# Optimization experiments

Measured on AMD Instinct MI355X. Metric: run time of the kernel, lower is better.

The kernel has to match this reference:

```python
import jax, jax.numpy as jnp
import numpy as np

N = 12288
E = 196608
H = 128
Z = 128
NEG = -1e9  # finite mask value (avoids -inf NaNs in grads)
WSCALE = 0.05


def setup_inputs() -> dict:
    key = jax.random.key(0)
    ks = jax.random.split(key, 16)
    inp = {}
    inp["x"] = jax.random.normal(ks[0], (N, 2), dtype=jnp.float32)
    inp["z"] = jax.random.normal(ks[1], (Z,), dtype=jnp.float32)
    inp["node_type"] = jax.random.randint(ks[2], (N,), 0, 3, dtype=jnp.int32)
    inp["node_depth"] = jax.random.randint(ks[3], (N,), 0, 64, dtype=jnp.int32)
    inp["edge_index"] = jax.random.randint(ks[4], (2, E), 0, N, dtype=jnp.int32)
    inp["W1"] = jax.random.normal(ks[5], (2, H), dtype=jnp.float32) * WSCALE
    inp["b1"] = jnp.zeros((H,), jnp.float32)
    inp["W2"] = jax.random.normal(ks[6], (H, H), dtype=jnp.float32) * WSCALE
    inp["b2"] = jnp.zeros((H,), jnp.float32)
    inp["Wm1"] = jax.random.normal(ks[7], (H + Z, H), dtype=jnp.float32) * WSCALE
    inp["bm1"] = jnp.zeros((H,), jnp.float32)
    inp["Wm2"] = jax.random.normal(ks[8], (H, H), dtype=jnp.float32) * WSCALE
    inp["bm2"] = jnp.zeros((H,), jnp.float32)
    inp["Ws"] = jax.random.normal(ks[9], (H, H), dtype=jnp.float32) * WSCALE
    inp["Wt"] = jax.random.normal(ks[10], (H, H), dtype=jnp.float32) * WSCALE
    inp["Wi1"] = jax.random.normal(ks[11], (2 * H + Z, H), dtype=jnp.float32) * WSCALE
    inp["bi1"] = jnp.zeros((H,), jnp.float32)
    inp["Wi2"] = jax.random.normal(ks[12], (H, 1), dtype=jnp.float32) * WSCALE
    inp["bi2"] = jnp.zeros((1,), jnp.float32)
    return inp


def _gcn(x, W, b, src, dst, n):
    # GCNConv with self-loops and symmetric deg^-1/2 normalization
    loop = jnp.arange(n, dtype=src.dtype)
    s = jnp.concatenate([src, loop])
    d = jnp.concatenate([dst, loop])
    deg = jax.ops.segment_sum(jnp.ones_like(d, dtype=x.dtype), d, num_segments=n)
    inv_sqrt = jnp.where(deg > 0, jax.lax.rsqrt(jnp.maximum(deg, 1.0)), 0.0)
    w = inv_sqrt[s] * inv_sqrt[d]  # [E+N]
    agg = jax.ops.segment_sum(x[s] * w[:, None], d, num_segments=n)  # [N,F]
    return agg @ W + b


def reference(x, z, node_type, node_depth, edge_index,
              W1, b1, W2, b2, Wm1, bm1, Wm2, bm2, Ws, Wt, Wi1, bi1, Wi2, bi2):
    n = x.shape[0]
    src, dst = edge_index[0], edge_index[1]
    # 2-layer GCN encode
    h = jax.nn.relu(_gcn(x, W1, b1, src, dst, n))
    h = jax.nn.relu(_gcn(h, W2, b2, src, dst, n))
    # node_mlp on [h, z] (no outer relu, per original edge_index branch)
    zb = jnp.broadcast_to(z, (n, Z))
    h = jax.nn.relu(jnp.concatenate([h, zb], axis=1) @ Wm1 + bm1) @ Wm2 + bm2  # [N,H]
    # batched score: St[v,u] = tgt_proj(h_v) . src_proj(h_u)
    St = (h @ Wt) @ (h @ Ws).T  # [N(target), N(candidate)]
    cand_ok = node_depth[None, :] < node_depth[:, None]  # candidate strictly shallower
    St = jnp.where(cand_ok, St, NEG)
    vals, idx = jax.lax.top_k(St, 2)  # [N,2] per-target top candidates
    # target is active if type != 0, depth > 0, and at least one candidate exists
    tv = (node_type != 0) & (node_depth > 0) & (vals[:, 0] > NEG / 2)
    # k=2 edges for AND nodes (type==2), else k=1
    edge_valid = jnp.stack([tv, tv & (node_type == 2)], axis=1)  # [N,2]
    # inversion bit mlp on [h_u, h_v, z]
    hu = h[idx]  # [N,2,H]
    hv = jnp.broadcast_to(h[:, None, :], hu.shape)
    zz = jnp.broadcast_to(z, (n, 2, Z))
    feat = jnp.concatenate([hu, hv, zz], axis=-1)  # [N,2,2H+Z]
    logit = (jax.nn.relu(feat @ Wi1 + bi1) @ Wi2 + bi2)[..., 0]  # [N,2]
    inv_prob = jax.nn.sigmoid(logit)
    return inv_prob, vals, idx, edge_valid
```

## Files before the change

### kernel.cpp

```cpp
#include <hip/hip_runtime.h>
#include <hip/hip_bf16.h>

#define NN 12288
#define NE 196608
#define HD 128
#define ZD 128
#define NEGV (-1.0e9f)
#define SEG 16

using s8v = __attribute__((ext_vector_type(8))) short;
using f4v = __attribute__((ext_vector_type(4))) float;
using i4v = __attribute__((ext_vector_type(4))) int;

__device__ __forceinline__ unsigned short f2bf(float f) {
    return __builtin_bit_cast(unsigned short, __float2bfloat16(f));
}
__device__ __forceinline__ float4 pack8(float4 a, float4 b) {
    unsigned p0 = ((unsigned)f2bf(a.y) << 16) | f2bf(a.x);
    unsigned p1 = ((unsigned)f2bf(a.w) << 16) | f2bf(a.z);
    unsigned p2 = ((unsigned)f2bf(b.y) << 16) | f2bf(b.x);
    unsigned p3 = ((unsigned)f2bf(b.w) << 16) | f2bf(b.z);
    i4v r = (i4v){(int)p0, (int)p1, (int)p2, (int)p3};
    return __builtin_bit_cast(float4, r);
}
// ... 126 lines not shown
    __shared__ int lh[64];
    __shared__ int lbase[64];
    int tid = threadIdx.x;
    if (blockIdx.x < NE / 256) {
        int e = blockIdx.x * 256 + tid;
        int u = esrc[e], v = edst[e];
        int pos = atomicAdd(&cursor[v], 1);
        ebsrc[pos] = u;
        ebw[pos] = inv[u] * inv[v];
    } else {
        if (tid < 64) lh[tid] = 0;
        __syncthreads();
        int v = (blockIdx.x - NE / 256) * 256 + tid;
        int d = ndep[v];
        int r = atomicAdd(&lh[d], 1);
        __syncthreads();
        if (tid < 64) {
            int c = lh[tid];
            if (c) lbase[tid] = atomicAdd(&dcur[tid * 16], c);
        }
        __syncthreads();
        int p = lbase[d] + r;
        sidx[p] = v;
        sdep[p] = d;
        prank[v] = p;
    }
}

__global__ __launch_bounds__(256) void k_gather2(const int* __restrict__ offs,
                                                 const int* __restrict__ ebsrc,
                                                 const float* __restrict__ ebw,
                                                 const float* __restrict__ x,
                                                 float* agg2) {
    int v = blockIdx.x * 256 + threadIdx.x;
    float ax = agg2[2 * v], ay = agg2[2 * v + 1];
    int b = offs[v], e = offs[v + 1];
    const float2* X2 = (const float2*)x;
    int k = b;
    for (; k + 4 <= e; k += 4) {
        int u0 = ebsrc[k], u1 = ebsrc[k + 1], u2 = ebsrc[k + 2], u3 = ebsrc[k + 3];
        float w0 = ebw[k], w1 = ebw[k + 1], w2 = ebw[k + 2], w3 = ebw[k + 3];
        float2 x0 = X2[u0], x1 = X2[u1], x2 = X2[u2], x3 = X2[u3];
        ax = fmaf(x0.x, w0, ax); ay = fmaf(x0.y, w0, ay);
        ax = fmaf(x1.x, w1, ax); ay = fmaf(x1.y, w1, ay);
        ax = fmaf(x2.x, w2, ax); ay = fmaf(x2.y, w2, ay);
        ax = fmaf(x3.x, w3, ax); ay = fmaf(x3.y, w3, ay);
    }
    for (; k < e; ++k) {
        int u = ebsrc[k];
        float w = ebw[k];
        float2 xv = X2[u];
        ax = fmaf(xv.x, w, ax);
        ay = fmaf(xv.y, w, ay);
    }
    agg2[2 * v] = ax;
    agg2[2 * v + 1] = ay;
}

__global__ __launch_bounds__(256) void k_lin1(const float* __restrict__ agg2,
                                              const float* __restrict__ W1,
                                              const float* __restrict__ b1,
                                              const float* __restrict__ inv,
                                              unsigned short* h1b, float* aggH) {
    int t = blockIdx.x * 256 + threadIdx.x;
    int v = t >> 7, j = t & 127;
    float hv = fmaxf(fmaf(agg2[2 * v], W1[j],
                     fmaf(agg2[2 * v + 1], W1[HD + j], b1[j])), 0.f);
    h1b[t] = f2bf(hv);
    float iv = inv[v];
    aggH[t] = hv * iv * iv;
}

__global__ __launch_bounds__(256) void k_gatherH(const int* __restrict__ offs,
                                                 const int* __restrict__ ebsrc,
                                                 const float* __restrict__ ebw,
                                                 const unsigned short* __restrict__ h1b,
                                                 float* aggH) {
    int tid = threadIdx.x;
    int lane = tid & 63;
    int v = blockIdx.x * 4 + (tid >> 6);
    const unsigned* H1 = (const unsigned*)h1b;
    float2* A2 = (float2*)aggH;
    float2 acc = A2[(size_t)v * 64 + lane];
    int b = offs[v], e = offs[v + 1];
    int k = b;
    for (; k + 4 <= e; k += 4) {
        int u0 = ebsrc[k], u1 = ebsrc[k + 1], u2 = ebsrc[k + 2], u3 = ebsrc[k + 3];
        float w0 = ebw[k], w1 = ebw[k + 1], w2 = ebw[k + 2], w3 = ebw[k + 3];
        unsigned hb0 = H1[(size_t)u0 * 64 + lane];
// ... 108 lines not shown
        const float4* wt = wt4 + 2 * 2048;
        NBACC(wt, col0, cA) NBACC(wt, col1, cB)
        float q0 = bbm2[col0], q1 = bbm2[col1];
        LDS4(cA, q0, col0, usB) LDS4(cB, q1, col1, usB)
    }
    __syncthreads();
    {
        AFRAGS(bufB4)
        const float4* wt = wt4 + 3 * 2048;
        NBACC(wt, col0, cA) NBACC(wt, col1, cB)
        GBF4S(cA, col0, htb) GBF4S(cB, col1, htb)
    }
    {
        AFRAGS(bufB4)
        const float4* wt = wt4 + 4 * 2048;
        NBACC(wt, col0, cA) NBACC(wt, col1, cB)
        GBF4S(cA, col0, hsb) GBF4S(cB, col1, hsb)
    }
    {
        AFRAGS(bufB4)
        const float4* wt = wt4 + 5 * 2048;
        NBACC(wt, col0, cA) NBACC(wt, col1, cB)
        GF4(cA, 0.f, col0, outA) GF4(cB, 0.f, col1, outA)
    }
    {
        AFRAGS(bufB4)
        const float4* wt = wt4 + 6 * 2048;
        NBACC(wt, col0, cA) NBACC(wt, col1, cB)
        float q0 = bcz2[col0], q1 = bcz2[col1];
        GF4(cA, q0, col0, outB) GF4(cB, q1, col1, outB)
    }
}

#define STG(buf, q, val) { int r_ = (q) >> 4, c_ = (q) & 15; \
    (buf)[r_ * 16 + (c_ ^ (r_ & 7))] = (val); }

#define KC2(kc, AX, AY) { \
    int co_ = (kc) * 4 + quad; \
    int bo_ = bbase + (co_ ^ brm); \
    s8v b0_ = __builtin_bit_cast(s8v, B[bo_      ]); \
    s8v b1_ = __builtin_bit_cast(s8v, B[bo_ + 256]); \
    s8v b2_ = __builtin_bit_cast(s8v, B[bo_ + 512]); \
    s8v b3_ = __builtin_bit_cast(s8v, B[bo_ + 768]); \
    x0 = __builtin_amdgcn_mfma_f32_16x16x32_bf16(AX, b0_, x0, 0, 0, 0); \
    y0 = __builtin_amdgcn_mfma_f32_16x16x32_bf16(AY, b0_, y0, 0, 0, 0); \
    x1 = __builtin_amdgcn_mfma_f32_16x16x32_bf16(AX, b1_, x1, 0, 0, 0); \
    y1 = __builtin_amdgcn_mfma_f32_16x16x32_bf16(AY, b1_, y1, 0, 0, 0); \
    x2 = __builtin_amdgcn_mfma_f32_16x16x32_bf16(AX, b2_, x2, 0, 0, 0); \
    y2 = __builtin_amdgcn_mfma_f32_16x16x32_bf16(AY, b2_, y2, 0, 0, 0); \
    x3 = __builtin_amdgcn_mfma_f32_16x16x32_bf16(AX, b3_, x3, 0, 0, 0); \
    y3 = __builtin_amdgcn_mfma_f32_16x16x32_bf16(AY, b3_, y3, 0, 0, 0); }

#define RMG(K1, K2, EL, DV) { \
    unsigned pb_ = (__builtin_bit_cast(unsigned, EL) & 0xFFFFC000u) | e_; \
    float sf_ = __builtin_bit_cast(float, (du_ < (DV)) ? pb_ : negp_); \
    K2 = __builtin_amdgcn_fmed3f(K1, K2, sf_); \
    K1 = fmaxf(K1, sf_); }

#define MGEN(nb, XA, YA) { \
    int p_ = u0 + (nb) * 16 + lane16; \
    int du_ = sdep[p_]; \
    unsigned e_ = 0x3FFFu - (unsigned)sidx[p_]; \
    unsigned negp_ = negbase | e_; \
    RMG(k1x0, k2x0, XA[0], dvx0) RMG(k1x1, k2x1, XA[1], dvx1) \
    RMG(k1x2, k2x2, XA[2], dvx2) RMG(k1x3, k2x3, XA[3], dvx3) \
    RMG(k1y0, k2y0, YA[0], dvy0) RMG(k1y1, k2y1, YA[1], dvy1) \
    RMG(k1y2, k2y2, YA[2], dvy2) RMG(k1y3, k2y3, YA[3], dvy3) }

#define RMF(K1, K2, EL) { \
    float sf_ = __builtin_bit_cast(float, \
        (__builtin_bit_cast(unsigned, EL) & 0xFFFFC000u) | e_); \
    K2 = __builtin_amdgcn_fmed3f(K1, K2, sf_); \
    K1 = fmaxf(K1, sf_); }

#define MFAST(nb, XA, YA) { \
    int p_ = u0 + (nb) * 16 + lane16; \
    unsigned e_ = 0x3FFFu - (unsigned)sidx[p_]; \
    RMF(k1x0, k2x0, XA[0]) RMF(k1x1, k2x1, XA[1]) \
    RMF(k1x2, k2x2, XA[2]) RMF(k1x3, k2x3, XA[3]) \
    RMF(k1y0, k2y0, YA[0]) RMF(k1y1, k2y1, YA[1]) \
    RMF(k1y2, k2y2, YA[2]) RMF(k1y3, k2y3, YA[3]) }

#define BF1(K1, K2, m) { \
    float o1_ = __shfl_xor(K1, m, 64); \
    float o2_ = __shfl_xor(K2, m, 64); \
    float m2_ = fmaxf(K2, o2_); \
    K2 = __builtin_amdgcn_fmed3f(K1, o1_, m2_); \
    K1 = fmaxf(K1, o1_); }

#define BFALL(m) \
    BF1(k1x0, k2x0, m) BF1(k1x1, k2x1, m) BF1(k1x2, k2x2, m) BF1(k1x3, k2x3, m) \
    BF1(k1y0, k2y0, m) BF1(k1y1, k2y1, m) BF1(k1y2, k2y2, m) BF1(k1y3, k2y3, m)

#define EMIT2(K1, K2, GROW) { \
    size_t o = ((size_t)seg * NN + (GROW)) * 2; \
    pv[o] = K1; pv[o + 1] = K2; }

__global__ __launch_bounds__(256) void k_score_top2_mfma(
        const __hip_bfloat16* __restrict__ htb,
        const __hip_bfloat16* __restrict__ hsb,
        const int* __restrict__ sdep, const int* __restrict__ sidx,
        const int* __restrict__ bofs,
        float* __restrict__ pv) {
    __shared__ float4 Bs4[2][64 * 16];
    int tid = threadIdx.x;
    int w = tid >> 6;
    int l = tid & 63;
    int lane16 = l & 15;
    int quad = l >> 4;
    int rb = (int)gridDim.x - 1 - (int)blockIdx.x;
    int row0 = rb * 128;
    int seg = blockIdx.y;
    const unsigned negbase = __builtin_bit_cast(unsigned, NEGV) & 0xFFFFC000u;

    int dmax = sdep[row0 + 127];
    int lim = bofs[dmax];
    int nt = (lim + 63) >> 6;
    int ns = (nt + 11) / 12;
    if (ns < 1) ns = 1;
    if (seg >= ns) {
        if (tid < 128) {
            int grow = sidx[row0 + tid];
            size_t o = ((size_t)seg * NN + grow) * 2;
            pv[o]     = __builtin_bit_cast(float, negbase | 0x3FFFu);
            pv[o + 1] = __builtin_bit_cast(float, negbase | 0x3FFEu);
        }
        return;
    }
    int t0 = (seg * nt) / ns;
    int t1 = ((seg + 1) * nt) / ns;

    int rbase = row0 + w * 32;
    s8v ax0, ax1, ax2, ax3, ay0, ay1, ay2, ay3;
    {
        const float4* gx = (const float4*)(htb + (size_t)(rbase + lane16) * HD);
        ax0 = __builtin_bit_cast(s8v, gx[quad]);
        ax1 = __builtin_bit_cast(s8v, gx[4 + quad]);
        ax2 = __builtin_bit_cast(s8v, gx[8 + quad]);
        ax3 = __builtin_bit_cast(s8v, gx[12 + quad]);
        const float4* gy = (const float4*)(htb + (size_t)(rbase + 16 + lane16) * HD);
        ay0 = __builtin_bit_cast(s8v, gy[quad]);
        ay1 = __builtin_bit_cast(s8v, gy[4 + quad]);
        ay2 = __builtin_bit_cast(s8v, gy[8 + quad]);
        ay3 = __builtin_bit_cast(s8v, gy[12 + quad]);
    }
    if (t0 < t1) {
        float4* B0 = Bs4[t0 & 1];
        const float4* gb = (const float4*)(hsb + (size_t)(t0 * 64) * HD);
        float4 b0_ = gb[tid], b1_ = gb[tid + 256], b2_ = gb[tid + 512], b3_ = gb[tid + 768];
        STG(B0, tid, b0_) STG(B0, tid + 256, b1_)
        STG(B0, tid + 512, b2_) STG(B0, tid + 768, b3_)
    }

    int bbase = lane16 * 16, brm = lane16 & 7;

    int dvx0 = sdep[rbase + quad * 4 + 0];
    int dvx1 = sdep[rbase + quad * 4 + 1];
    int dvx2 = sdep[rbase + quad * 4 + 2];
    int dvx3 = sdep[rbase + quad * 4 + 3];
    int dvy0 = sdep[rbase + 16 + quad * 4 + 0];
    int dvy1 = sdep[rbase + 16 + quad * 4 + 1];
    int dvy2 = sdep[rbase + 16 + quad * 4 + 2];
    int dvy3 = sdep[rbase + 16 + quad * 4 + 3];
    int lim_lo = bofs[sdep[rbase]];
    int lim_hi = bofs[sdep[rbase + 31]];

    float ki1 = (lane16 == 0) ? __builtin_bit_cast(float, negbase | 0x3FFFu) : -3.4e38f;
    float ki2 = (lane16 == 0) ? __builtin_bit_cast(float, negbase | 0x3FFEu) : -3.4e38f;
    float k1x0 = ki1, k1x1 = ki1, k1x2 = ki1, k1x3 = ki1;
    float k1y0 = ki1, k1y1 = ki1, k1y2 = ki1, k1y3 = ki1;
    float k2x0 = ki2, k2x1 = ki2, k2x2 = ki2, k2x3 = ki2;
    float k2y0 = ki2, k2y1 = ki2, k2y2 = ki2, k2y3 = ki2;

    float4 p0, p1, p2, p3;
    for (int t = t0; t < t1; ++t) {
        int u0 = t * 64;
        __syncthreads();
        if (t + 1 < t1) {
            const float4* g = (const float4*)(hsb + (size_t)(u0 + 64) * HD);
            p0 = g[tid]; p1 = g[tid + 256]; p2 = g[tid + 512]; p3 = g[tid + 768];
        }
        if (u0 < lim_hi) {
            const float4* B = Bs4[t & 1];
            f4v x0 = (f4v){0.f, 0.f, 0.f, 0.f};
            f4v x1 = (f4v){0.f, 0.f, 0.f, 0.f};
            f4v x2 = (f4v){0.f, 0.f, 0.f, 0.f};
            f4v x3 = (f4v){0.f, 0.f, 0.f, 0.f};
            f4v y0 = (f4v){0.f, 0.f, 0.f, 0.f};
            f4v y1 = (f4v){0.f, 0.f, 0.f, 0.f};
            f4v y2 = (f4v){0.f, 0.f, 0.f, 0.f};
            f4v y3 = (f4v){0.f, 0.f, 0.f, 0.f};
            KC2(0, ax0, ay0) KC2(1, ax1, ay1) KC2(2, ax2, ay2) KC2(3, ax3, ay3)
            if (u0 + 64 <= lim_lo) {
                MFAST(0, x0, y0) MFAST(1, x1, y1)
                MFAST(2, x2, y2) MFAST(3, x3, y3)
            } else {
                MGEN(0, x0, y0) MGEN(1, x1, y1)
                MGEN(2, x2, y2) MGEN(3, x3, y3)
            }
        }
        if (t + 1 < t1) {
            float4* Bn = Bs4[(t + 1) & 1];
            STG(Bn, tid, p0) STG(Bn, tid + 256, p1)
            STG(Bn, tid + 512, p2) STG(Bn, tid + 768, p3)
        }
    }

    BFALL(1) BFALL(2) BFALL(4) BFALL(8)

    if (lane16 == 0) {
        int gbse = rbase + quad * 4;
        EMIT2(k1x0, k2x0, sidx[gbse + 0])
        EMIT2(k1x1, k2x1, sidx[gbse + 1])
        EMIT2(k1x2, k2x2, sidx[gbse + 2])
        EMIT2(k1x3, k2x3, sidx[gbse + 3])
        EMIT2(k1y0, k2y0, sidx[gbse + 16])
        EMIT2(k1y1, k2y1, sidx[gbse + 17])
        EMIT2(k1y2, k2y2, sidx[gbse + 18])
        EMIT2(k1y3, k2y3, sidx[gbse + 19])
    }
}

__global__ __launch_bounds__(256) void k_final(const float* __restrict__ pv,
                                               const int* __restrict__ ntype,
                                               const int* __restrict__ ndepth,
                                               const float* __restrict__ A,
                                               const float* __restrict__ B,
                                               const float* __restrict__ Wi2,
                                               const float* __restrict__ bi2,
                                               float* __restrict__ out) {
    int tid = threadIdx.x;
    int lane = tid & 63;
    int v = blockIdx.x * 4 + (tid >> 6);

    float k1 = -3.4e38f;
    if (lane < 32) {
        k1 = pv[((size_t)(lane >> 1) * NN + v) * 2 + (lane & 1)];
    }
    float k2 = -3.4e38f;
#pragma unroll
    for (int m = 1; m <= 16; m <<= 1) {
        float o1 = __shfl_xor(k1, m, 64);
        float o2 = __shfl_xor(k2, m, 64);
        float m2 = fmaxf(k2, o2);
        k2 = __builtin_amdgcn_fmed3f(k1, o1, m2);
        k1 = fmaxf(k1, o1);
    }
    float K1 = __shfl(k1, 0, 64);
    float K2 = __shfl(k2, 0, 64);
    unsigned b1 = __builtin_bit_cast(unsigned, K1);
    unsigned b2 = __builtin_bit_cast(unsigned, K2);
    int I1 = 0x3FFF - (int)(b1 & 0x3FFFu);
// ... 67 lines not shown
    int*   pi     = (int*)(pv + S2N);
    int*   cnt    = pi;
    int*   dcur   = pi + 1024;
    int*   degi   = pi + S2N;
    float* inv    = (float*)(degi + NN + 64);
    float* agg2   = inv + NN;
    float* cz1    = agg2 + 2 * NN;
    float* cz2    = cz1 + 128;
    int*   offs   = (int*)(cz2 + 128);
    int*   cursor = offs + NN + 16;
    int*   bofs   = cursor + NN;
    int*   sidx   = bofs + 80 + 64;
    int*   sdep   = sidx + NN;
    int*   prank  = sdep + NN;
    int*   ebsrc  = prank + NN;
    float* ebw    = (float*)(ebsrc + NE);
    __hip_bfloat16* wt7 = (__hip_bfloat16*)(ebw + NE);
    size_t F = (size_t)NN * HD;
    float* s0 = (float*)(wt7 + 7 * 16384);
    float* s1 = s0 + F;
    float* s2 = s1 + F;
    unsigned short* h1b = (unsigned short*)s0;
    __hip_bfloat16* htb = (__hip_bfloat16*)s0;
    __hip_bfloat16* hsb = htb + F;

    hipMemsetAsync(degi, 0, NN * sizeof(int), stream);
    hipMemsetAsync(cnt, 0, 1024 * sizeof(int), stream);
    k_counts_wz<<<NE / 256 + NN / 256 + 448 + 1, 256, 0, stream>>>(
        edst, ndep, W2, Wm1, Wm2, Wtm, Wsm, Wi1, z, bm1, bi1,
        degi, cnt, wt7, cz1, cz2);
    k_prefix<<<1, 1024, 0, stream>>>(degi, cnt, x, inv, agg2, offs, cursor, bofs, dcur);
    k_bucket_scatter<<<NE / 256 + NN / 256, 256, 0, stream>>>(
        esrc, edst, ndep, inv, cursor, ebsrc, ebw, dcur, sidx, sdep, prank);
    k_gather2<<<NN / 256, 256, 0, stream>>>(offs, ebsrc, ebw, x, agg2);
    k_lin1<<<NN * HD / 256, 256, 0, stream>>>(agg2, W1, b1, inv, h1b, s1);
    k_gatherH<<<NN / 4, 256, 0, stream>>>(offs, ebsrc, ebw, h1b, s1);
    k_mlp7_mfma<<<NN / 16, 256, 0, stream>>>(s1, wt7, b2, cz1, bm2, cz2,
                                             prank, s2, s1, htb, hsb);
    k_score_top2_mfma<<<dim3(NN / 128, SEG), 256, 0, stream>>>(
        htb, hsb, sdep, sidx, bofs, pv);
    k_final<<<NN / 4, 256, 0, stream>>>(pv, ntype, ndep, s2, s1, Wi2, bi2, out);
}
```

Baseline: 229.2 us.

## Double rows per wave in score/top2 kernel and stage candidate depth/index in LDS

Each wave of the score-and-top-2 kernel now handles 64 target rows instead of 32, so each block covers 256 rows and the grid halves. Every candidate B fragment read from shared memory now feeds twice as many MFMAs, cutting LDS traffic per unit of work. Candidate depth and index are also packed once per segment into a shared array, replacing the global sdep/sidx reads done inside the merge loop. The cost is roughly double the accumulator and top-2 register state, which may lower occupancy or cause spills, and fewer blocks in the grid.

Result: slower. 254.0 us (+10.8%).

```diff
diff --git a/kernel.cpp b/kernel.cpp
--- a/kernel.cpp
+++ b/kernel.cpp
@@ -382,21 +382,29 @@
 #define STG(buf, q, val) { int r_ = (q) >> 4, c_ = (q) & 15; \
     (buf)[r_ * 16 + (c_ ^ (r_ & 7))] = (val); }
 
-#define KC2(kc, AX, AY) { \
+#define MFMA_ __builtin_amdgcn_mfma_f32_16x16x32_bf16
+
+#define KC4(kc, AA, AB, AC, AD) { \
     int co_ = (kc) * 4 + quad; \
     int bo_ = bbase + (co_ ^ brm); \
     s8v b0_ = __builtin_bit_cast(s8v, B[bo_      ]); \
     s8v b1_ = __builtin_bit_cast(s8v, B[bo_ + 256]); \
     s8v b2_ = __builtin_bit_cast(s8v, B[bo_ + 512]); \
     s8v b3_ = __builtin_bit_cast(s8v, B[bo_ + 768]); \
-    x0 = __builtin_amdgcn_mfma_f32_16x16x32_bf16(AX, b0_, x0, 0, 0, 0); \
-    y0 = __builtin_amdgcn_mfma_f32_16x16x32_bf16(AY, b0_, y0, 0, 0, 0); \
-    x1 = __builtin_amdgcn_mfma_f32_16x16x32_bf16(AX, b1_, x1, 0, 0, 0); \
-    y1 = __builtin_amdgcn_mfma_f32_16x16x32_bf16(AY, b1_, y1, 0, 0, 0); \
-    x2 = __builtin_amdgcn_mfma_f32_16x16x32_bf16(AX, b2_, x2, 0, 0, 0); \
-    y2 = __builtin_amdgcn_mfma_f32_16x16x32_bf16(AY, b2_, y2, 0, 0, 0); \
-    x3 = __builtin_amdgcn_mfma_f32_16x16x32_bf16(AX, b3_, x3, 0, 0, 0); \
-    y3 = __builtin_amdgcn_mfma_f32_16x16x32_bf16(AY, b3_, y3, 0, 0, 0); }
+    accA0 = MFMA_(AA, b0_, accA0, 0, 0, 0); accB0 = MFMA_(AB, b0_, accB0, 0, 0, 0); \
+    accC0 = MFMA_(AC, b0_, accC0, 0, 0, 0); accD0 = MFMA_(AD, b0_, accD0, 0, 0, 0); \
+    accA1 = MFMA_(AA, b1_, accA1, 0, 0, 0); accB1 = MFMA_(AB, b1_, accB1, 0, 0, 0); \
+    accC1 = MFMA_(AC, b1_, accC1, 0, 0, 0); accD1 = MFMA_(AD, b1_, accD1, 0, 0, 0); \
+    accA2 = MFMA_(AA, b2_, accA2, 0, 0, 0); accB2 = MFMA_(AB, b2_, accB2, 0, 0, 0); \
+    accC2 = MFMA_(AC, b2_, accC2, 0, 0, 0); accD2 = MFMA_(AD, b2_, accD2, 0, 0, 0); \
+    accA3 = MFMA_(AA, b3_, accA3, 0, 0, 0); accB3 = MFMA_(AB, b3_, accB3, 0, 0, 0); \
+    accC3 = MFMA_(AC, b3_, accC3, 0, 0, 0); accD3 = MFMA_(AD, b3_, accD3, 0, 0, 0); }
+
+#define RMF(K1, K2, EL) { \
+    float sf_ = __builtin_bit_cast(float, \
+        (__builtin_bit_cast(unsigned, EL) & 0xFFFFC000u) | e_); \
+    K2 = __builtin_amdgcn_fmed3f(K1, K2, sf_); \
+    K1 = fmaxf(K1, sf_); }
 
 #define RMG(K1, K2, EL, DV) { \
     unsigned pb_ = (__builtin_bit_cast(unsigned, EL) & 0xFFFFC000u) | e_; \
@@ -404,29 +412,24 @@
     K2 = __builtin_amdgcn_fmed3f(K1, K2, sf_); \
     K1 = fmaxf(K1, sf_); }
 
-#define MGEN(nb, XA, YA) { \
-    int p_ = u0 + (nb) * 16 + lane16; \
-    int du_ = sdep[p_]; \
-    unsigned e_ = 0x3FFFu - (unsigned)sidx[p_]; \
+#define RMF4(G, NB) \
+    RMF(k1##G##0, k2##G##0, acc##G##NB[0]) RMF(k1##G##1, k2##G##1, acc##G##NB[1]) \
+    RMF(k1##G##2, k2##G##2, acc##G##NB[2]) RMF(k1##G##3, k2##G##3, acc##G##NB[3])
+
+#define RMG4(G, NB) \
+    RMG(k1##G##0, k2##G##0, acc##G##NB[0], dv##G##0) RMG(k1##G##1, k2##G##1, acc##G##NB[1], dv##G##1) \
+    RMG(k1##G##2, k2##G##2, acc##G##NB[2], dv##G##2) RMG(k1##G##3, k2##G##3, acc##G##NB[3], dv##G##3)
+
+#define MFAST(NB) { \
+    unsigned e_ = eds[ebase + (NB) * 16 + lane16] & 0x3FFFu; \
+    RMF4(A, NB) RMF4(B, NB) RMF4(C, NB) RMF4(D, NB) }
+
+#define MGEN(NB) { \
+    unsigned pk_ = eds[ebase + (NB) * 16 + lane16]; \
+    int du_ = (int)(pk_ >> 16); \
+    unsigned e_ = pk_ & 0x3FFFu; \
     unsigned negp_ = negbase | e_; \
-    RMG(k1x0, k2x0, XA[0], dvx0) RMG(k1x1, k2x1, XA[1], dvx1) \
-    RMG(k1x2, k2x2, XA[2], dvx2) RMG(k1x3, k2x3, XA[3], dvx3) \
-    RMG(k1y0, k2y0, YA[0], dvy0) RMG(k1y1, k2y1, YA[1], dvy1) \
-    RMG(k1y2, k2y2, YA[2], dvy2) RMG(k1y3, k2y3, YA[3], dvy3) }
-
-#define RMF(K1, K2, EL) { \
-    float sf_ = __builtin_bit_cast(float, \
-        (__builtin_bit_cast(unsigned, EL) & 0xFFFFC000u) | e_); \
-    K2 = __builtin_amdgcn_fmed3f(K1, K2, sf_); \
-    K1 = fmaxf(K1, sf_); }
-
-#define MFAST(nb, XA, YA) { \
-    int p_ = u0 + (nb) * 16 + lane16; \
-    unsigned e_ = 0x3FFFu - (unsigned)sidx[p_]; \
-    RMF(k1x0, k2x0, XA[0]) RMF(k1x1, k2x1, XA[1]) \
-    RMF(k1x2, k2x2, XA[2]) RMF(k1x3, k2x3, XA[3]) \
-    RMF(k1y0, k2y0, YA[0]) RMF(k1y1, k2y1, YA[1]) \
-    RMF(k1y2, k2y2, YA[2]) RMF(k1y3, k2y3, YA[3]) }
+    RMG4(A, NB) RMG4(B, NB) RMG4(C, NB) RMG4(D, NB) }
 
 #define BF1(K1, K2, m) { \
     float o1_ = __shfl_xor(K1, m, 64); \
@@ -435,13 +438,19 @@
     K2 = __builtin_amdgcn_fmed3f(K1, o1_, m2_); \
     K1 = fmaxf(K1, o1_); }
 
-#define BFALL(m) \
-    BF1(k1x0, k2x0, m) BF1(k1x1, k2x1, m) BF1(k1x2, k2x2, m) BF1(k1x3, k2x3, m) \
-    BF1(k1y0, k2y0, m) BF1(k1y1, k2y1, m) BF1(k1y2, k2y2, m) BF1(k1y3, k2y3, m)
+#define BF4(G, m) \
+    BF1(k1##G##0, k2##G##0, m) BF1(k1##G##1, k2##G##1, m) \
+    BF1(k1##G##2, k2##G##2, m) BF1(k1##G##3, k2##G##3, m)
+
+#define BFALLv(m) BF4(A, m) BF4(B, m) BF4(C, m) BF4(D, m)
 
 #define EMIT2(K1, K2, GROW) { \
     size_t o = ((size_t)seg * NN + (GROW)) * 2; \
     pv[o] = K1; pv[o + 1] = K2; }
+
+#define EM4(G, OFF) { int gb_ = rbase + (OFF) + quad * 4; \
+    EMIT2(k1##G##0, k2##G##0, sidx[gb_ + 0]) EMIT2(k1##G##1, k2##G##1, sidx[gb_ + 1]) \
+    EMIT2(k1##G##2, k2##G##2, sidx[gb_ + 2]) EMIT2(k1##G##3, k2##G##3, sidx[gb_ + 3]) }
 
 __global__ __launch_bounds__(256) void k_score_top2_mfma(
         const __hip_bfloat16* __restrict__ htb,
@@ -450,46 +459,60 @@
         const int* __restrict__ bofs,
         float* __restrict__ pv) {
     __shared__ float4 Bs4[2][64 * 16];
+    __shared__ unsigned eds[12 * 64];
     int tid = threadIdx.x;
     int w = tid >> 6;
     int l = tid & 63;
     int lane16 = l & 15;
     int quad = l >> 4;
     int rb = (int)gridDim.x - 1 - (int)blockIdx.x;
-    int row0 = rb * 128;
+    int row0 = rb * 256;
     int seg = blockIdx.y;
     const unsigned negbase = __builtin_bit_cast(unsigned, NEGV) & 0xFFFFC000u;
 
-    int dmax = sdep[row0 + 127];
+    int dmax = sdep[row0 + 255];
     int lim = bofs[dmax];
     int nt = (lim + 63) >> 6;
     int ns = (nt + 11) / 12;
     if (ns < 1) ns = 1;
     if (seg >= ns) {
-        if (tid < 128) {
-            int grow = sidx[row0 + tid];
-            size_t o = ((size_t)seg * NN + grow) * 2;
-            pv[o]     = __builtin_bit_cast(float, negbase | 0x3FFFu);
-            pv[o + 1] = __builtin_bit_cast(float, negbase | 0x3FFEu);
-        }
+        int grow = sidx[row0 + tid];
+        size_t o = ((size_t)seg * NN + grow) * 2;
+        pv[o]     = __builtin_bit_cast(float, negbase | 0x3FFFu);
+        pv[o + 1] = __builtin_bit_cast(float, negbase | 0x3FFEu);
         return;
     }
     int t0 = (seg * nt) / ns;
     int t1 = ((seg + 1) * nt) / ns;
 
-    int rbase = row0 + w * 32;
-    s8v ax0, ax1, ax2, ax3, ay0, ay1, ay2, ay3;
-    {
-        const float4* gx = (const float4*)(htb + (size_t)(rbase + lane16) * HD);
-        ax0 = __builtin_bit_cast(s8v, gx[quad]);
-        ax1 = __builtin_bit_cast(s8v, gx[4 + quad]);
-        ax2 = __builtin_bit_cast(s8v, gx[8 + quad]);
-        ax3 = __builtin_bit_cast(s8v, gx[12 + quad]);
-        const float4* gy = (const float4*)(htb + (size_t)(rbase + 16 + lane16) * HD);
-        ay0 = __builtin_bit_cast(s8v, gy[quad]);
-        ay1 = __builtin_bit_cast(s8v, gy[4 + quad]);
-        ay2 = __builtin_bit_cast(s8v, gy[8 + quad]);
-        ay3 = __builtin_bit_cast(s8v, gy[12 + quad]);
+    int rbase = row0 + w * 64;
+    s8v aA0, aA1, aA2, aA3, aB0, aB1, aB2, aB3;
+    s8v aC0, aC1, aC2, aC3, aD0, aD1, aD2, aD3;
+    {
+        const float4* g_ = (const float4*)(htb + (size_t)(rbase + lane16) * HD);
+        aA0 = __builtin_bit_cast(s8v, g_[quad]);
+        aA1 = __builtin_bit_cast(s8v, g_[4 + quad]);
+        aA2 = __builtin_bit_cast(s8v, g_[8 + quad]);
+        aA3 = __builtin_bit_cast(s8v, g_[12 + quad]);
+        g_ = (const float4*)(htb + (size_t)(rbase + 16 + lane16) * HD);
+        aB0 = __builtin_bit_cast(s8v, g_[quad]);
+        aB1 = __builtin_bit_cast(s8v, g_[4 + quad]);
+        aB2 = __builtin_bit_cast(s8v, g_[8 + quad]);
+        aB3 = __builtin_bit_cast(s8v, g_[12 + quad]);
+        g_ = (const float4*)(htb + (size_t)(rbase + 32 + lane16) * HD);
+        aC0 = __builtin_bit_cast(s8v, g_[quad]);
+        aC1 = __builtin_bit_cast(s8v, g_[4 + quad]);
+        aC2 = __builtin_bit_cast(s8v, g_[8 + quad]);
+        aC3 = __builtin_bit_cast(s8v, g_[12 + quad]);
+        g_ = (const float4*)(htb + (size_t)(rbase + 48 + lane16) * HD);
+        aD0 = __builtin_bit_cast(s8v, g_[quad]);
+        aD1 = __builtin_bit_cast(s8v, g_[4 + quad]);
+        aD2 = __builtin_bit_cast(s8v, g_[8 + quad]);
+        aD3 = __builtin_bit_cast(s8v, g_[12 + quad]);
+    }
+    for (int i = tid; i < (t1 - t0) * 64; i += 256) {
+        int p = t0 * 64 + i;
+        eds[i] = ((unsigned)sdep[p] << 16) | (0x3FFFu - (unsigned)sidx[p]);
     }
     if (t0 < t1) {
         float4* B0 = Bs4[t0 & 1];
@@ -501,27 +524,40 @@
 
     int bbase = lane16 * 16, brm = lane16 & 7;
 
-    int dvx0 = sdep[rbase + quad * 4 + 0];
-    int dvx1 = sdep[rbase + quad * 4 + 1];
-    int dvx2 = sdep[rbase + quad * 4 + 2];
-    int dvx3 = sdep[rbase + quad * 4 + 3];
-    int dvy0 = sdep[rbase + 16 + quad * 4 + 0];
-    int dvy1 = sdep[rbase + 16 + quad * 4 + 1];
-    int dvy2 = sdep[rbase + 16 + quad * 4 + 2];
-    int dvy3 = sdep[rbase + 16 + quad * 4 + 3];
+    int dvA0 = sdep[rbase + quad * 4 + 0];
+    int dvA1 = sdep[rbase + quad * 4 + 1];
+    int dvA2 = sdep[rbase + quad * 4 + 2];
+    int dvA3 = sdep[rbase + quad * 4 + 3];
+    int dvB0 = sdep[rbase + 16 + quad * 4 + 0];
+    int dvB1 = sdep[rbase + 16 + quad * 4 + 1];
+    int dvB2 = sdep[rbase + 16 + quad * 4 + 2];
+    int dvB3 = sdep[rbase + 16 + quad * 4 + 3];
+    int dvC0 = sdep[rbase + 32 + quad * 4 + 0];
+    int dvC1 = sdep[rbase + 32 + quad * 4 + 1];
+    int dvC2 = sdep[rbase + 32 + quad * 4 + 2];
+    int dvC3 = sdep[rbase + 32 + quad * 4 + 3];
+    int dvD0 = sdep[rbase + 48 + quad * 4 + 0];
+    int dvD1 = sdep[rbase + 48 + quad * 4 + 1];
+    int dvD2 = sdep[rbase + 48 + quad * 4 + 2];
+    int dvD3 = sdep[rbase + 48 + quad * 4 + 3];
     int lim_lo = bofs[sdep[rbase]];
-    int lim_hi = bofs[sdep[rbase + 31]];
+    int lim_hi = bofs[sdep[rbase + 63]];
 
     float ki1 = (lane16 == 0) ? __builtin_bit_cast(float, negbase | 0x3FFFu) : -3.4e38f;
     float ki2 = (lane16 == 0) ? __builtin_bit_cast(float, negbase | 0x3FFEu) : -3.4e38f;
-    float k1x0 = ki1, k1x1 = ki1, k1x2 = ki1, k1x3 = ki1;
-    float k1y0 = ki1, k1y1 = ki1, k1y2 = ki1, k1y3 = ki1;
-    float k2x0 = ki2, k2x1 = ki2, k2x2 = ki2, k2x3 = ki2;
-    float k2y0 = ki2, k2y1 = ki2, k2y2 = ki2, k2y3 = ki2;
+    float k1A0 = ki1, k1A1 = ki1, k1A2 = ki1, k1A3 = ki1;
+    float k1B0 = ki1, k1B1 = ki1, k1B2 = ki1, k1B3 = ki1;
+    float k1C0 = ki1, k1C1 = ki1, k1C2 = ki1, k1C3 = ki1;
+    float k1D0 = ki1, k1D1 = ki1, k1D2 = ki1, k1D3 = ki1;
+    float k2A0 = ki2, k2A1 = ki2, k2A2 = ki2, k2A3 = ki2;
+    float k2B0 = ki2, k2B1 = ki2, k2B2 = ki2, k2B3 = ki2;
+    float k2C0 = ki2, k2C1 = ki2, k2C2 = ki2, k2C3 = ki2;
+    float k2D0 = ki2, k2D1 = ki2, k2D2 = ki2, k2D3 = ki2;
 
     float4 p0, p1, p2, p3;
     for (int t = t0; t < t1; ++t) {
         int u0 = t * 64;
+        int ebase = (t - t0) * 64;
         __syncthreads();
         if (t + 1 < t1) {
             const float4* g = (const float4*)(hsb + (size_t)(u0 + 64) * HD);
@@ -529,21 +565,20 @@
         }
         if (u0 < lim_hi) {
             const float4* B = Bs4[t & 1];
-            f4v x0 = (f4v){0.f, 0.f, 0.f, 0.f};
-            f4v x1 = (f4v){0.f, 0.f, 0.f, 0.f};
-            f4v x2 = (f4v){0.f, 0.f, 0.f, 0.f};
-            f4v x3 = (f4v){0.f, 0.f, 0.f, 0.f};
-            f4v y0 = (f4v){0.f, 0.f, 0.f, 0.f};
-            f4v y1 = (f4v){0.f, 0.f, 0.f, 0.f};
-            f4v y2 = (f4v){0.f, 0.f, 0.f, 0.f};
-            f4v y3 = (f4v){0.f, 0.f, 0.f, 0.f};
-            KC2(0, ax0, ay0) KC2(1, ax1, ay1) KC2(2, ax2, ay2) KC2(3, ax3, ay3)
+            f4v accA0 = (f4v){0.f,0.f,0.f,0.f}, accA1 = (f4v){0.f,0.f,0.f,0.f};
+            f4v accA2 = (f4v){0.f,0.f,0.f,0.f}, accA3 = (f4v){0.f,0.f,0.f,0.f};
+            f4v accB0 = (f4v){0.f,0.f,0.f,0.f}, accB1 = (f4v){0.f,0.f,0.f,0.f};
+            f4v accB2 = (f4v){0.f,0.f,0.f,0.f}, accB3 = (f4v){0.f,0.f,0.f,0.f};
+            f4v accC0 = (f4v){0.f,0.f,0.f,0.f}, accC1 = (f4v){0.f,0.f,0.f,0.f};
+            f4v accC2 = (f4v){0.f,0.f,0.f,0.f}, accC3 = (f4v){0.f,0.f,0.f,0.f};
+            f4v accD0 = (f4v){0.f,0.f,0.f,0.f}, accD1 = (f4v){0.f,0.f,0.f,0.f};
+            f4v accD2 = (f4v){0.f,0.f,0.f,0.f}, accD3 = (f4v){0.f,0.f,0.f,0.f};
+            KC4(0, aA0, aB0, aC0, aD0) KC4(1, aA1, aB1, aC1, aD1)
+            KC4(2, aA2, aB2, aC2, aD2) KC4(3, aA3, aB3, aC3, aD3)
             if (u0 + 64 <= lim_lo) {
-                MFAST(0, x0, y0) MFAST(1, x1, y1)
-                MFAST(2, x2, y2) MFAST(3, x3, y3)
+                MFAST(0) MFAST(1) MFAST(2) MFAST(3)
             } else {
-                MGEN(0, x0, y0) MGEN(1, x1, y1)
-                MGEN(2, x2, y2) MGEN(3, x3, y3)
+                MGEN(0) MGEN(1) MGEN(2) MGEN(3)
             }
         }
         if (t + 1 < t1) {
@@ -553,18 +588,10 @@
         }
     }
 
-    BFALL(1) BFALL(2) BFALL(4) BFALL(8)
+    BFALLv(1) BFALLv(2) BFALLv(4) BFALLv(8)
 
     if (lane16 == 0) {
-        int gbse = rbase + quad * 4;
-        EMIT2(k1x0, k2x0, sidx[gbse + 0])
-        EMIT2(k1x1, k2x1, sidx[gbse + 1])
-        EMIT2(k1x2, k2x2, sidx[gbse + 2])
-        EMIT2(k1x3, k2x3, sidx[gbse + 3])
-        EMIT2(k1y0, k2y0, sidx[gbse + 16])
-        EMIT2(k1y1, k2y1, sidx[gbse + 17])
-        EMIT2(k1y2, k2y2, sidx[gbse + 18])
-        EMIT2(k1y3, k2y3, sidx[gbse + 19])
+        EM4(A, 0) EM4(B, 16) EM4(C, 32) EM4(D, 48)
     }
 }
 
@@ -703,7 +730,7 @@
     k_gatherH<<<NN / 4, 256, 0, stream>>>(offs, ebsrc, ebw, h1b, s1);
     k_mlp7_mfma<<<NN / 16, 256, 0, stream>>>(s1, wt7, b2, cz1, bm2, cz2,
                                              prank, s2, s1, htb, hsb);
-    k_score_top2_mfma<<<dim3(NN / 128, SEG), 256, 0, stream>>>(
+    k_score_top2_mfma<<<dim3(NN / 256, SEG), 256, 0, stream>>>(
         htb, hsb, sdep, sidx, bofs, pv);
     k_final<<<NN / 4, 256, 0, stream>>>(pv, ntype, ndep, s2, s1, Wi2, bi2, out);
 }
```

## Load score B tiles directly from global memory instead of LDS double buffer

Applied to the files above, without the earlier changes.

Removes the shared-memory double-buffered staging of candidate h_s tiles, so each wave reads its B fragments straight from global memory (through L1/L2) in the MFMA loop. This drops the per-tile __syncthreads and the LDS stores and loads, and lets each wave break early once its candidates pass the depth limit. In exchange, the four waves of a block each load the same B tile separately, raising global/L2 traffic and exposing load latency without explicit prefetching.

After: 317.0 us. 38.3% more time.

```diff
diff --git a/kernel.cpp b/kernel.cpp
--- a/kernel.cpp
+++ b/kernel.cpp
@@ -379,24 +379,17 @@
     }
 }
 
-#define STG(buf, q, val) { int r_ = (q) >> 4, c_ = (q) & 15; \
-    (buf)[r_ * 16 + (c_ ^ (r_ & 7))] = (val); }
-
-#define KC2(kc, AX, AY) { \
-    int co_ = (kc) * 4 + quad; \
-    int bo_ = bbase + (co_ ^ brm); \
-    s8v b0_ = __builtin_bit_cast(s8v, B[bo_      ]); \
-    s8v b1_ = __builtin_bit_cast(s8v, B[bo_ + 256]); \
-    s8v b2_ = __builtin_bit_cast(s8v, B[bo_ + 512]); \
-    s8v b3_ = __builtin_bit_cast(s8v, B[bo_ + 768]); \
-    x0 = __builtin_amdgcn_mfma_f32_16x16x32_bf16(AX, b0_, x0, 0, 0, 0); \
-    y0 = __builtin_amdgcn_mfma_f32_16x16x32_bf16(AY, b0_, y0, 0, 0, 0); \
-    x1 = __builtin_amdgcn_mfma_f32_16x16x32_bf16(AX, b1_, x1, 0, 0, 0); \
-    y1 = __builtin_amdgcn_mfma_f32_16x16x32_bf16(AY, b1_, y1, 0, 0, 0); \
-    x2 = __builtin_amdgcn_mfma_f32_16x16x32_bf16(AX, b2_, x2, 0, 0, 0); \
-    y2 = __builtin_amdgcn_mfma_f32_16x16x32_bf16(AY, b2_, y2, 0, 0, 0); \
-    x3 = __builtin_amdgcn_mfma_f32_16x16x32_bf16(AX, b3_, x3, 0, 0, 0); \
-    y3 = __builtin_amdgcn_mfma_f32_16x16x32_bf16(AY, b3_, y3, 0, 0, 0); }
+#define MFMA_ __builtin_amdgcn_mfma_f32_16x16x32_bf16
+
+#define KCG(kc, AX, AY) { \
+    s8v b0_ = __builtin_bit_cast(s8v, gB[(kc) * 4 + quad      ]); \
+    s8v b1_ = __builtin_bit_cast(s8v, gB[(kc) * 4 + quad + 256]); \
+    s8v b2_ = __builtin_bit_cast(s8v, gB[(kc) * 4 + quad + 512]); \
+    s8v b3_ = __builtin_bit_cast(s8v, gB[(kc) * 4 + quad + 768]); \
+    x0 = MFMA_(AX, b0_, x0, 0, 0, 0); y0 = MFMA_(AY, b0_, y0, 0, 0, 0); \
+    x1 = MFMA_(AX, b1_, x1, 0, 0, 0); y1 = MFMA_(AY, b1_, y1, 0, 0, 0); \
+    x2 = MFMA_(AX, b2_, x2, 0, 0, 0); y2 = MFMA_(AY, b2_, y2, 0, 0, 0); \
+    x3 = MFMA_(AX, b3_, x3, 0, 0, 0); y3 = MFMA_(AY, b3_, y3, 0, 0, 0); }
 
 #define RMG(K1, K2, EL, DV) { \
     unsigned pb_ = (__builtin_bit_cast(unsigned, EL) & 0xFFFFC000u) | e_; \
@@ -449,7 +442,6 @@
         const int* __restrict__ sdep, const int* __restrict__ sidx,
         const int* __restrict__ bofs,
         float* __restrict__ pv) {
-    __shared__ float4 Bs4[2][64 * 16];
     int tid = threadIdx.x;
     int w = tid >> 6;
     int l = tid & 63;
@@ -491,15 +483,6 @@
         ay2 = __builtin_bit_cast(s8v, gy[8 + quad]);
         ay3 = __builtin_bit_cast(s8v, gy[12 + quad]);
     }
-    if (t0 < t1) {
-        float4* B0 = Bs4[t0 & 1];
-        const float4* gb = (const float4*)(hsb + (size_t)(t0 * 64) * HD);
-        float4 b0_ = gb[tid], b1_ = gb[tid + 256], b2_ = gb[tid + 512], b3_ = gb[tid + 768];
-        STG(B0, tid, b0_) STG(B0, tid + 256, b1_)
-        STG(B0, tid + 512, b2_) STG(B0, tid + 768, b3_)
-    }
-
-    int bbase = lane16 * 16, brm = lane16 & 7;
 
     int dvx0 = sdep[rbase + quad * 4 + 0];
     int dvx1 = sdep[rbase + quad * 4 + 1];
@@ -519,37 +502,25 @@
     float k2x0 = ki2, k2x1 = ki2, k2x2 = ki2, k2x3 = ki2;
     float k2y0 = ki2, k2y1 = ki2, k2y2 = ki2, k2y3 = ki2;
 
-    float4 p0, p1, p2, p3;
     for (int t = t0; t < t1; ++t) {
         int u0 = t * 64;
-        __syncthreads();
-        if (t + 1 < t1) {
-            const float4* g = (const float4*)(hsb + (size_t)(u0 + 64) * HD);
-            p0 = g[tid]; p1 = g[tid + 256]; p2 = g[tid + 512]; p3 = g[tid + 768];
-        }
-        if (u0 < lim_hi) {
-            const float4* B = Bs4[t & 1];
-            f4v x0 = (f4v){0.f, 0.f, 0.f, 0.f};
-            f4v x1 = (f4v){0.f, 0.f, 0.f, 0.f};
-            f4v x2 = (f4v){0.f, 0.f, 0.f, 0.f};
-            f4v x3 = (f4v){0.f, 0.f, 0.f, 0.f};
-            f4v y0 = (f4v){0.f, 0.f, 0.f, 0.f};
-            f4v y1 = (f4v){0.f, 0.f, 0.f, 0.f};
-            f4v y2 = (f4v){0.f, 0.f, 0.f, 0.f};
-            f4v y3 = (f4v){0.f, 0.f, 0.f, 0.f};
-            KC2(0, ax0, ay0) KC2(1, ax1, ay1) KC2(2, ax2, ay2) KC2(3, ax3, ay3)
-            if (u0 + 64 <= lim_lo) {
-                MFAST(0, x0, y0) MFAST(1, x1, y1)
-                MFAST(2, x2, y2) MFAST(3, x3, y3)
-            } else {
-                MGEN(0, x0, y0) MGEN(1, x1, y1)
-                MGEN(2, x2, y2) MGEN(3, x3, y3)
-            }
-        }
-        if (t + 1 < t1) {
-            float4* Bn = Bs4[(t + 1) & 1];
-            STG(Bn, tid, p0) STG(Bn, tid + 256, p1)
-            STG(Bn, tid + 512, p2) STG(Bn, tid + 768, p3)
+        if (u0 >= lim_hi) break;
+        const float4* gB = (const float4*)(hsb + (size_t)(u0 + lane16) * HD);
+        f4v x0 = (f4v){0.f, 0.f, 0.f, 0.f};
+        f4v x1 = (f4v){0.f, 0.f, 0.f, 0.f};
+        f4v x2 = (f4v){0.f, 0.f, 0.f, 0.f};
+        f4v x3 = (f4v){0.f, 0.f, 0.f, 0.f};
+        f4v y0 = (f4v){0.f, 0.f, 0.f, 0.f};
+        f4v y1 = (f4v){0.f, 0.f, 0.f, 0.f};
+        f4v y2 = (f4v){0.f, 0.f, 0.f, 0.f};
+        f4v y3 = (f4v){0.f, 0.f, 0.f, 0.f};
+        KCG(0, ax0, ay0) KCG(1, ax1, ay1) KCG(2, ax2, ay2) KCG(3, ax3, ay3)
+        if (u0 + 64 <= lim_lo) {
+            MFAST(0, x0, y0) MFAST(1, x1, y1)
+            MFAST(2, x2, y2) MFAST(3, x3, y3)
+        } else {
+            MGEN(0, x0, y0) MGEN(1, x1, y1)
+            MGEN(2, x2, y2) MGEN(3, x3, y3)
         }
     }
 
```

## Split score kernel columns across 8 waves and parallelize edge gather per node

Applied to the files above, without the earlier changes.

The score/top-2 kernel now runs 512 threads per block, with wave pairs splitting each 64-column tile in half so each wave does half the MFMAs and top-2 updates per tile. The two partial top-2 results are merged through shared memory before the cross-lane reduction. Separately, the GCN degree-2 gather assigns 8 lanes per node with a shuffle reduction instead of one thread per node, to spread load from uneven degrees. The changes add an extra block-wide barrier and LDS merge, and put more register pressure on a 512-thread block.

After: 234.7 us. 1.02x slower.

```diff
diff --git a/kernel.cpp b/kernel.cpp
--- a/kernel.cpp
+++ b/kernel.cpp
@@ -182,29 +182,30 @@
                                                  const float* __restrict__ ebw,
                                                  const float* __restrict__ x,
                                                  float* agg2) {
-    int v = blockIdx.x * 256 + threadIdx.x;
-    float ax = agg2[2 * v], ay = agg2[2 * v + 1];
+    int t = blockIdx.x * 256 + threadIdx.x;
+    int v = t >> 3;
+    int sl = t & 7;
     int b = offs[v], e = offs[v + 1];
     const float2* X2 = (const float2*)x;
-    int k = b;
-    for (; k + 4 <= e; k += 4) {
-        int u0 = ebsrc[k], u1 = ebsrc[k + 1], u2 = ebsrc[k + 2], u3 = ebsrc[k + 3];
-        float w0 = ebw[k], w1 = ebw[k + 1], w2 = ebw[k + 2], w3 = ebw[k + 3];
-        float2 x0 = X2[u0], x1 = X2[u1], x2 = X2[u2], x3 = X2[u3];
-        ax = fmaf(x0.x, w0, ax); ay = fmaf(x0.y, w0, ay);
-        ax = fmaf(x1.x, w1, ax); ay = fmaf(x1.y, w1, ay);
-        ax = fmaf(x2.x, w2, ax); ay = fmaf(x2.y, w2, ay);
-        ax = fmaf(x3.x, w3, ax); ay = fmaf(x3.y, w3, ay);
-    }
-    for (; k < e; ++k) {
+    float ax = 0.f, ay = 0.f;
+    for (int k = b + sl; k < e; k += 8) {
         int u = ebsrc[k];
         float w = ebw[k];
         float2 xv = X2[u];
         ax = fmaf(xv.x, w, ax);
         ay = fmaf(xv.y, w, ay);
     }
-    agg2[2 * v] = ax;
-    agg2[2 * v + 1] = ay;
+#pragma unroll
+    for (int m = 1; m < 8; m <<= 1) {
+        ax += __shfl_xor(ax, m, 64);
+        ay += __shfl_xor(ay, m, 64);
+    }
+    if (sl == 0) {
+        float2* A2 = (float2*)agg2;
+        float2 cur = A2[v];
+        cur.x += ax; cur.y += ay;
+        A2[v] = cur;
+    }
 }
 
 __global__ __launch_bounds__(256) void k_lin1(const float* __restrict__ agg2,
@@ -382,21 +383,15 @@
 #define STG(buf, q, val) { int r_ = (q) >> 4, c_ = (q) & 15; \
     (buf)[r_ * 16 + (c_ ^ (r_ & 7))] = (val); }
 
+#define MFMA_ __builtin_amdgcn_mfma_f32_16x16x32_bf16
+
 #define KC2(kc, AX, AY) { \
     int co_ = (kc) * 4 + quad; \
-    int bo_ = bbase + (co_ ^ brm); \
+    int bo_ = bbase + (co_ ^ brm) + nbb * 256; \
     s8v b0_ = __builtin_bit_cast(s8v, B[bo_      ]); \
     s8v b1_ = __builtin_bit_cast(s8v, B[bo_ + 256]); \
-    s8v b2_ = __builtin_bit_cast(s8v, B[bo_ + 512]); \
-    s8v b3_ = __builtin_bit_cast(s8v, B[bo_ + 768]); \
-    x0 = __builtin_amdgcn_mfma_f32_16x16x32_bf16(AX, b0_, x0, 0, 0, 0); \
-    y0 = __builtin_amdgcn_mfma_f32_16x16x32_bf16(AY, b0_, y0, 0, 0, 0); \
-    x1 = __builtin_amdgcn_mfma_f32_16x16x32_bf16(AX, b1_, x1, 0, 0, 0); \
-    y1 = __builtin_amdgcn_mfma_f32_16x16x32_bf16(AY, b1_, y1, 0, 0, 0); \
-    x2 = __builtin_amdgcn_mfma_f32_16x16x32_bf16(AX, b2_, x2, 0, 0, 0); \
-    y2 = __builtin_amdgcn_mfma_f32_16x16x32_bf16(AY, b2_, y2, 0, 0, 0); \
-    x3 = __builtin_amdgcn_mfma_f32_16x16x32_bf16(AX, b3_, x3, 0, 0, 0); \
-    y3 = __builtin_amdgcn_mfma_f32_16x16x32_bf16(AY, b3_, y3, 0, 0, 0); }
+    x0 = MFMA_(AX, b0_, x0, 0, 0, 0); y0 = MFMA_(AY, b0_, y0, 0, 0, 0); \
+    x1 = MFMA_(AX, b1_, x1, 0, 0, 0); y1 = MFMA_(AY, b1_, y1, 0, 0, 0); }
 
 #define RMG(K1, K2, EL, DV) { \
     unsigned pb_ = (__builtin_bit_cast(unsigned, EL) & 0xFFFFC000u) | e_; \
@@ -405,7 +400,7 @@
     K1 = fmaxf(K1, sf_); }
 
 #define MGEN(nb, XA, YA) { \
-    int p_ = u0 + (nb) * 16 + lane16; \
+    int p_ = u0 + (nbb + (nb)) * 16 + lane16; \
     int du_ = sdep[p_]; \
     unsigned e_ = 0x3FFFu - (unsigned)sidx[p_]; \
     unsigned negp_ = negbase | e_; \
@@ -421,7 +416,7 @@
     K1 = fmaxf(K1, sf_); }
 
 #define MFAST(nb, XA, YA) { \
-    int p_ = u0 + (nb) * 16 + lane16; \
+    int p_ = u0 + (nbb + (nb)) * 16 + lane16; \
     unsigned e_ = 0x3FFFu - (unsigned)sidx[p_]; \
     RMF(k1x0, k2x0, XA[0]) RMF(k1x1, k2x1, XA[1]) \
     RMF(k1x2, k2x2, XA[2]) RMF(k1x3, k2x3, XA[3]) \
@@ -439,11 +434,16 @@
     BF1(k1x0, k2x0, m) BF1(k1x1, k2x1, m) BF1(k1x2, k2x2, m) BF1(k1x3, k2x3, m) \
     BF1(k1y0, k2y0, m) BF1(k1y1, k2y1, m) BF1(k1y2, k2y2, m) BF1(k1y3, k2y3, m)
 
+#define MRG(K1, K2, O1, O2) { \
+    float m2_ = fmaxf(K2, (O2)); \
+    K2 = __builtin_amdgcn_fmed3f(K1, (O1), m2_); \
+    K1 = fmaxf(K1, (O1)); }
+
 #define EMIT2(K1, K2, GROW) { \
     size_t o = ((size_t)seg * NN + (GROW)) * 2; \
     pv[o] = K1; pv[o + 1] = K2; }
 
-__global__ __launch_bounds__(256) void k_score_top2_mfma(
+__global__ __launch_bounds__(512) void k_score_top2_mfma(
         const __hip_bfloat16* __restrict__ htb,
         const __hip_bfloat16* __restrict__ hsb,
         const int* __restrict__ sdep, const int* __restrict__ sidx,
@@ -455,6 +455,9 @@
     int l = tid & 63;
     int lane16 = l & 15;
     int quad = l >> 4;
+    int rh = w >> 1;
+    int ch = w & 1;
+    int nbb = ch * 2;
     int rb = (int)gridDim.x - 1 - (int)blockIdx.x;
     int row0 = rb * 128;
     int seg = blockIdx.y;
@@ -477,7 +480,7 @@
     int t0 = (seg * nt) / ns;
     int t1 = ((seg + 1) * nt) / ns;
 
-    int rbase = row0 + w * 32;
+    int rbase = row0 + rh * 32;
     s8v ax0, ax1, ax2, ax3, ay0, ay1, ay2, ay3;
     {
         const float4* gx = (const float4*)(htb + (size_t)(rbase + lane16) * HD);
@@ -494,9 +497,8 @@
     if (t0 < t1) {
         float4* B0 = Bs4[t0 & 1];
         const float4* gb = (const float4*)(hsb + (size_t)(t0 * 64) * HD);
-        float4 b0_ = gb[tid], b1_ = gb[tid + 256], b2_ = gb[tid + 512], b3_ = gb[tid + 768];
-        STG(B0, tid, b0_) STG(B0, tid + 256, b1_)
-        STG(B0, tid + 512, b2_) STG(B0, tid + 768, b3_)
+        float4 b0_ = gb[tid], b1_ = gb[tid + 512];
+        STG(B0, tid, b0_) STG(B0, tid + 512, b1_)
     }
 
     int bbase = lane16 * 16, brm = lane16 & 7;
@@ -512,59 +514,80 @@
     int lim_lo = bofs[sdep[rbase]];
     int lim_hi = bofs[sdep[rbase + 31]];
 
-    float ki1 = (lane16 == 0) ? __builtin_bit_cast(float, negbase | 0x3FFFu) : -3.4e38f;
-    float ki2 = (lane16 == 0) ? __builtin_bit_cast(float, negbase | 0x3FFEu) : -3.4e38f;
+    float ki1 = (ch == 0 && lane16 == 0)
+        ? __builtin_bit_cast(float, negbase | 0x3FFFu) : -3.4e38f;
+    float ki2 = (ch == 0 && lane16 == 0)
+        ? __builtin_bit_cast(float, negbase | 0x3FFEu) : -3.4e38f;
     float k1x0 = ki1, k1x1 = ki1, k1x2 = ki1, k1x3 = ki1;
     float k1y0 = ki1, k1y1 = ki1, k1y2 = ki1, k1y3 = ki1;
     float k2x0 = ki2, k2x1 = ki2, k2x2 = ki2, k2x3 = ki2;
     float k2y0 = ki2, k2y1 = ki2, k2y2 = ki2, k2y3 = ki2;
 
-    float4 p0, p1, p2, p3;
+    float4 p0, p1;
     for (int t = t0; t < t1; ++t) {
         int u0 = t * 64;
         __syncthreads();
         if (t + 1 < t1) {
             const float4* g = (const float4*)(hsb + (size_t)(u0 + 64) * HD);
-            p0 = g[tid]; p1 = g[tid + 256]; p2 = g[tid + 512]; p3 = g[tid + 768];
+            p0 = g[tid]; p1 = g[tid + 512];
         }
         if (u0 < lim_hi) {
             const float4* B = Bs4[t & 1];
             f4v x0 = (f4v){0.f, 0.f, 0.f, 0.f};
             f4v x1 = (f4v){0.f, 0.f, 0.f, 0.f};
-            f4v x2 = (f4v){0.f, 0.f, 0.f, 0.f};
-            f4v x3 = (f4v){0.f, 0.f, 0.f, 0.f};
             f4v y0 = (f4v){0.f, 0.f, 0.f, 0.f};
             f4v y1 = (f4v){0.f, 0.f, 0.f, 0.f};
-            f4v y2 = (f4v){0.f, 0.f, 0.f, 0.f};
-            f4v y3 = (f4v){0.f, 0.f, 0.f, 0.f};
             KC2(0, ax0, ay0) KC2(1, ax1, ay1) KC2(2, ax2, ay2) KC2(3, ax3, ay3)
             if (u0 + 64 <= lim_lo) {
                 MFAST(0, x0, y0) MFAST(1, x1, y1)
-                MFAST(2, x2, y2) MFAST(3, x3, y3)
             } else {
                 MGEN(0, x0, y0) MGEN(1, x1, y1)
-                MGEN(2, x2, y2) MGEN(3, x3, y3)
             }
         }
         if (t + 1 < t1) {
             float4* Bn = Bs4[(t + 1) & 1];
-            STG(Bn, tid, p0) STG(Bn, tid + 256, p1)
-            STG(Bn, tid + 512, p2) STG(Bn, tid + 768, p3)
-        }
-    }
-
-    BFALL(1) BFALL(2) BFALL(4) BFALL(8)
-
-    if (lane16 == 0) {
-        int gbse = rbase + quad * 4;
-        EMIT2(k1x0, k2x0, sidx[gbse + 0])
-        EMIT2(k1x1, k2x1, sidx[gbse + 1])
-        EMIT2(k1x2, k2x2, sidx[gbse + 2])
-        EMIT2(k1x3, k2x3, sidx[gbse + 3])
-        EMIT2(k1y0, k2y0, sidx[gbse + 16])
-        EMIT2(k1y1, k2y1, sidx[gbse + 17])
-        EMIT2(k1y2, k2y2, sidx[gbse + 18])
-        EMIT2(k1y3, k2y3, sidx[gbse + 19])
+            STG(Bn, tid, p0) STG(Bn, tid + 512, p1)
+        }
+    }
+
+    __syncthreads();
+    float* S = (float*)Bs4;
+    if (ch == 1) {
+        int base = rh * 1024 + l;
+        S[base +  0 * 64] = k1x0; S[base +  1 * 64] = k1x1;
+        S[base +  2 * 64] = k1x2; S[base +  3 * 64] = k1x3;
+        S[base +  4 * 64] = k1y0; S[base +  5 * 64] = k1y1;
+        S[base +  6 * 64] = k1y2; S[base +  7 * 64] = k1y3;
+        S[base +  8 * 64] = k2x0; S[base +  9 * 64] = k2x1;
+        S[base + 10 * 64] = k2x2; S[base + 11 * 64] = k2x3;
+        S[base + 12 * 64] = k2y0; S[base + 13 * 64] = k2y1;
+        S[base + 14 * 64] = k2y2; S[base + 15 * 64] = k2y3;
+    }
+    __syncthreads();
+    if (ch == 0) {
+        int base = rh * 1024 + l;
+        MRG(k1x0, k2x0, S[base +  0 * 64], S[base +  8 * 64])
+        MRG(k1x1, k2x1, S[base +  1 * 64], S[base +  9 * 64])
+        MRG(k1x2, k2x2, S[base +  2 * 64], S[base + 10 * 64])
+        MRG(k1x3, k2x3, S[base +  3 * 64], S[base + 11 * 64])
+        MRG(k1y0, k2y0, S[base +  4 * 64], S[base + 12 * 64])
+        MRG(k1y1, k2y1, S[base +  5 * 64], S[base + 13 * 64])
+        MRG(k1y2, k2y2, S[base +  6 * 64], S[base + 14 * 64])
+        MRG(k1y3, k2y3, S[base +  7 * 64], S[base + 15 * 64])
+
+        BFALL(1) BFALL(2) BFALL(4) BFALL(8)
+
+        if (lane16 == 0) {
+            int gbse = rbase + quad * 4;
+            EMIT2(k1x0, k2x0, sidx[gbse + 0])
+            EMIT2(k1x1, k2x1, sidx[gbse + 1])
+            EMIT2(k1x2, k2x2, sidx[gbse + 2])
+            EMIT2(k1x3, k2x3, sidx[gbse + 3])
+            EMIT2(k1y0, k2y0, sidx[gbse + 16])
+            EMIT2(k1y1, k2y1, sidx[gbse + 17])
+            EMIT2(k1y2, k2y2, sidx[gbse + 18])
+            EMIT2(k1y3, k2y3, sidx[gbse + 19])
+        }
     }
 }
 
@@ -698,12 +721,12 @@
     k_prefix<<<1, 1024, 0, stream>>>(degi, cnt, x, inv, agg2, offs, cursor, bofs, dcur);
     k_bucket_scatter<<<NE / 256 + NN / 256, 256, 0, stream>>>(
         esrc, edst, ndep, inv, cursor, ebsrc, ebw, dcur, sidx, sdep, prank);
-    k_gather2<<<NN / 256, 256, 0, stream>>>(offs, ebsrc, ebw, x, agg2);
+    k_gather2<<<NN * 8 / 256, 256, 0, stream>>>(offs, ebsrc, ebw, x, agg2);
     k_lin1<<<NN * HD / 256, 256, 0, stream>>>(agg2, W1, b1, inv, h1b, s1);
     k_gatherH<<<NN / 4, 256, 0, stream>>>(offs, ebsrc, ebw, h1b, s1);
     k_mlp7_mfma<<<NN / 16, 256, 0, stream>>>(s1, wt7, b2, cz1, bm2, cz2,
                                              prank, s2, s1, htb, hsb);
-    k_score_top2_mfma<<<dim3(NN / 128, SEG), 256, 0, stream>>>(
+    k_score_top2_mfma<<<dim3(NN / 128, SEG), 512, 0, stream>>>(
         htb, hsb, sdep, sidx, bofs, pv);
     k_final<<<NN / 4, 256, 0, stream>>>(pv, ntype, ndep, s2, s1, Wi2, bi2, out);
 }
```
